# Kernel optimization log

Measured on AMD Instinct MI355X. Metric: run time of the kernel, lower is better.

Reference implementation:

```python
import jax, jax.numpy as jnp
import numpy as np

B, T, V, E, H = 256, 512, 30000, 256, 32


def _run_dir(x, mask, Wih, Whh, bih, bhh, reverse):
    # x: [B,T,D], mask: [B,T] bool. PyTorch GRU gate order: r, z, n.
    gi = jnp.einsum('btd,gd->btg', x, Wih) + bih  # precompute input gates [B,T,3H]
    h0 = jnp.zeros((x.shape[0], Whh.shape[1]), x.dtype)

    def step(h, inp):
        gi_t, m_t = inp
        gh = h @ Whh.T + bhh
        ir, iz, inn = jnp.split(gi_t, 3, axis=-1)
        hr, hz, hn = jnp.split(gh, 3, axis=-1)
        r = jax.nn.sigmoid(ir + hr)
        z = jax.nn.sigmoid(iz + hz)
        n = jnp.tanh(inn + r * hn)
        h_new = (1.0 - z) * n + z * h
        # packed-sequence semantics: freeze state at padded steps
        h = jnp.where(m_t[:, None], h_new, h)
        return h, h

    hT, ys = jax.lax.scan(step, h0, (jnp.swapaxes(gi, 0, 1), mask.T), reverse=reverse)
    return jnp.swapaxes(ys, 0, 1), hT  # outputs [B,T,H], final hidden [B,H]


def _bigru_layer(x, mask, pf, pb):
    of, hf = _run_dir(x, mask, *pf, reverse=False)
    ob, hb = _run_dir(x, mask, *pb, reverse=True)
    return jnp.concatenate([of, ob], axis=-1), hf, hb


def setup_inputs() -> dict:
    key = jax.random.key(0)
    ks = jax.random.split(key, 24)
    lengths = jax.random.randint(ks[0], (B,), 1, T + 1)
    mask = (jnp.arange(T)[None, :] < lengths[:, None]).astype(jnp.int32)
    ids = jax.random.randint(ks[1], (B, T), 1, V)
    ids = jnp.where(mask > 0, ids, 0)  # pad_id = 0 at padded positions
    embed = (jax.random.normal(ks[2], (V, E), jnp.float32) * 0.1).at[0].set(0.0)

    def gru_params(k, din):
        k1, k2, k3, k4 = jax.random.split(k, 4)
        s = 1.0 / np.sqrt(H)
        return (jax.random.uniform(k1, (3 * H, din), jnp.float32, -s, s),
                jax.random.uniform(k2, (3 * H, H), jnp.float32, -s, s),
                jax.random.uniform(k3, (3 * H,), jnp.float32, -s, s),
                jax.random.uniform(k4, (3 * H,), jnp.float32, -s, s))

    inp = {"input_ids": ids, "attention_mask": mask, "embed": embed}
    i = 3
    for layer, din in (("l0", E), ("l1", 2 * H)):
        for d in ("f", "b"):
            Wih, Whh, bih, bhh = gru_params(ks[i], din); i += 1
            inp[f"Wih_{layer}{d}"] = Wih
            inp[f"Whh_{layer}{d}"] = Whh
            inp[f"bih_{layer}{d}"] = bih
            inp[f"bhh_{layer}{d}"] = bhh
    s = 1.0 / np.sqrt(2 * H)
    inp["Wout"] = jax.random.uniform(ks[i], (6, 2 * H), jnp.float32, -s, s)
    inp["bout"] = jax.random.uniform(ks[i + 1], (6,), jnp.float32, -s, s)
    return inp


def reference(input_ids, attention_mask, embed,
              Wih_l0f, Whh_l0f, bih_l0f, bhh_l0f,
              Wih_l0b, Whh_l0b, bih_l0b, bhh_l0b,
              Wih_l1f, Whh_l1f, bih_l1f, bhh_l1f,
              Wih_l1b, Whh_l1b, bih_l1b, bhh_l1b,
              Wout, bout):
    mask = attention_mask > 0
    x = embed[input_ids]  # [B,T,E]
    x1, _, _ = _bigru_layer(x, mask,
                            (Wih_l0f, Whh_l0f, bih_l0f, bhh_l0f),
                            (Wih_l0b, Whh_l0b, bih_l0b, bhh_l0b))
    # no dropout: eval-mode forward
    _, hf, hb = _bigru_layer(x1, mask,
                             (Wih_l1f, Whh_l1f, bih_l1f, bhh_l1f),
                             (Wih_l1b, Whh_l1b, bih_l1b, bhh_l1b))
    top = jnp.concatenate([hf, hb], axis=-1)  # h_n[-2:] -> [B, 2H]
    return top @ Wout.T + bout  # [B, 6]
```

## Files before the change

### kernel.cpp

```cpp
#include <hip/hip_runtime.h>
#include <hip/hip_bf16.h>
#include <stdint.h>

#define B_ 256
#define T_ 512
#define V_ 30000
#define E_ 256
#define H_ 32

typedef float v2f __attribute__((ext_vector_type(2)));
typedef unsigned int uint2e __attribute__((ext_vector_type(2)));

#define LOG2E_F 1.44269504088896340736f

__device__ __forceinline__ float exp2_fast(float x) {
    float r; asm("v_exp_f32 %0, %1" : "=v"(r) : "v"(x)); return r;
}
__device__ __forceinline__ float rcp_fast(float x) {
    float r; asm("v_rcp_f32 %0, %1" : "=v"(r) : "v"(x)); return r;
}
__device__ __forceinline__ void pk_fma(v2f& acc, v2f w, v2f h) {
    asm("v_pk_fma_f32 %0, %1, %2, %0" : "+v"(acc) : "v"(w), "v"(h));
}
template <int CTRL>
__device__ __forceinline__ float mdpp(float x) {
    return __int_as_float(
        __builtin_amdgcn_mov_dpp(__float_as_int(x), CTRL, 0xF, 0xF, true));
}
#define DPP_XOR1  0xB1
#define DPP_XOR2  0x4E
#define DPP_XOR3  0x1B
#define DPP_XOR7  0x141
#define DPP_XOR15 0x140

__device__ __forceinline__ float xsum32(float x) {
    uint2e r = __builtin_amdgcn_permlane32_swap(
        __float_as_uint(x), __float_as_uint(x), false, false);
    return __uint_as_float(r.x) + __uint_as_float(r.y);
}
__device__ __forceinline__ float swap16(float x) {
    uint2e r = __builtin_amdgcn_permlane16_swap(
        __float_as_uint(x), __float_as_uint(x), false, false);
    return __uint_as_float(r.x ^ r.y ^ __float_as_uint(x));
}

#define GEMM_MT 64
#define GEMM_KC 32
#define GEMM_PA 68
#define GEMM_PB 196

__global__ __launch_bounds__(256) void gemm_gates(
    const float* __restrict__ A, int M, int K,
    const float* __restrict__ Wf, const float* __restrict__ Wb,
    const float* __restrict__ bihf, const float* __restrict__ bhhf,
    const float* __restrict__ bihb, const float* __restrict__ bhhb,
    float* __restrict__ Out)
{
    __shared__ float As[GEMM_KC][GEMM_PA];
    __shared__ float Bs[GEMM_KC][GEMM_PB];

    const int tid = threadIdx.x;
    const int mbase = blockIdx.x * GEMM_MT;
    const int mg = tid >> 5, ng = tid & 31;
    const int m_off = mg * 8, n_off = ng * 6;

    float acc[8][6];
    #pragma unroll
    for (int r = 0; r < 8; ++r)
        #pragma unroll
        for (int c = 0; c < 6; ++c) acc[r][c] = 0.f;

    for (int kc = 0; kc < K; kc += GEMM_KC) {
        #pragma unroll
        for (int i = 0; i < 2; ++i) {
            int fi = tid + 256 * i;
            int row = fi >> 3, cf = fi & 7;
            int m = mbase + row;
            float4 v = make_float4(0.f, 0.f, 0.f, 0.f);
            if (m < M) v = *(const float4*)&A[(size_t)m * K + kc + cf * 4];
            As[cf * 4 + 0][row] = v.x; As[cf * 4 + 1][row] = v.y;
            As[cf * 4 + 2][row] = v.z; As[cf * 4 + 3][row] = v.w;
        }
        #pragma unroll
        for (int i = 0; i < 6; ++i) {
            int fi = tid + 256 * i;
            int g = fi >> 3, cf = fi & 7;
            const float* Wsel = (g < 96) ? (Wf + (size_t)g * K)
                                         : (Wb + (size_t)(g - 96) * K);
            float4 v = *(const float4*)&Wsel[kc + cf * 4];
            Bs[cf * 4 + 0][g] = v.x; Bs[cf * 4 + 1][g] = v.y;
            Bs[cf * 4 + 2][g] = v.z; Bs[cf * 4 + 3][g] = v.w;
        }
        __syncthreads();
        #pragma unroll
        for (int k = 0; k < GEMM_KC; ++k) {
            float a[8], bb[6];
            *(float4*)&a[0] = *(const float4*)&As[k][m_off];
            *(float4*)&a[4] = *(const float4*)&As[k][m_off + 4];
            *(float2*)&bb[0] = *(const float2*)&Bs[k][n_off];
            *(float2*)&bb[2] = *(const float2*)&Bs[k][n_off + 2];
            *(float2*)&bb[4] = *(const float2*)&Bs[k][n_off + 4];
            #pragma unroll
            for (int r = 0; r < 8; ++r)
                #pragma unroll
                for (int c = 0; c < 6; ++c)
                    acc[r][c] = fmaf(a[r], bb[c], acc[r][c]);
        }
        __syncthreads();
    }

    float bias[6], gsc[6];
    #pragma unroll
    for (int c = 0; c < 6; ++c) {
        int g = n_off + c;
        int g96 = (g < 96) ? g : g - 96;
        const float* bih = (g < 96) ? bihf : bihb;
        const float* bhh = (g < 96) ? bhhf : bhhb;
        bias[c] = bih[g96] + ((g96 < 64) ? bhh[g96] : 0.f);
        gsc[c]  = (g96 < 64) ? -LOG2E_F : 2.0f * LOG2E_F;
    }
    #pragma unroll
    for (int r = 0; r < 8; ++r) {
        int m = mbase + m_off + r;
        if (m < M) {
            float* op = &Out[(size_t)m * 192 + n_off];
            #pragma unroll
            for (int c = 0; c < 6; ++c) op[c] = (acc[r][c] + bias[c]) * gsc[c];
        }
    }
}

template <int USE_IDS>
__global__ __launch_bounds__(64, 1)
__attribute__((amdgpu_waves_per_eu(1, 1)))
void gru_scan(
    const float* __restrict__ gi,
    const int* __restrict__ ids,
    const int* __restrict__ mask,
    const float* __restrict__ Whh_f, const float* __restrict__ Whh_b,
    const float* __restrict__ bhh_f, const float* __restrict__ bhh_b,
    float* __restrict__ out_seq,
    float* __restrict__ out_fin)
{
    const int l = threadIdx.x;
    const int i16 = l & 15;
    const int row = l >> 4;
    const int hi = row & 1;
    const int kh = row >> 1;
    const int j = i16 + 16 * hi;
    const bool lower = l < 32;
    const bool self_seed = (hi == kh);
    const int dir = blockIdx.x & 1;
    const int b = blockIdx.x >> 1;
    const int bT = b * T_;

    const float* Whh = dir ? Whh_b : Whh_f;
    const float* bhh = dir ? bhh_b : bhh_f;

    const float sRZ = -LOG2E_F;
    const float sN2 = 2.0f * LOG2E_F;

    const int M0[8] = {0, 2, 7, 5, 15, 13, 8, 10};
    const int M1[8] = {1, 3, 6, 4, 14, 12, 9, 11};

    v2f wR[8], wZ[8], wN[8];
    #pragma unroll
    for (int q = 0; q < 8; ++q) {
        const int c0 = kh * 16 + (i16 ^ M0[q]);
        const int c1 = kh * 16 + (i16 ^ M1[q]);
        wR[q] = (v2f){Whh[j * 32 + c0] * sRZ, Whh[j * 32 + c1] * sRZ};
        wZ[q] = (v2f){Whh[(32 + j) * 32 + c0] * sRZ,
                      Whh[(32 + j) * 32 + c1] * sRZ};
        wN[q] = (v2f){Whh[(64 + j) * 32 + c0] * sN2,
                      Whh[(64 + j) * 32 + c1] * sN2};
    }
    float bns = bhh[64 + j] * sN2;

    #pragma unroll
    for (int q = 0; q < 8; ++q)
        asm volatile("" : "+v"(wR[q]), "+v"(wZ[q]), "+v"(wN[q]));
    asm volatile("" : "+v"(bns));

    const int offR = dir * 96 + j;

    auto t_of = [&](int n) { return dir ? (T_ - 1 - n) : n; };
    auto cbase = [&](int c) { return dir ? (bT + 510 - 2 * c) : (bT + 2 * c); };

    int mk_cur = lower ? mask[bT + t_of(l)] : 0;
    int mk_nxt = lower ? mask[bT + t_of(32 + l)] : 0;

    int2 ids_pf = make_int2(0, 0), ids_in = make_int2(0, 0);
    float gR[2][2], gZ[2][2], gN[2][2];
    {
        int ra, rb;
        if (USE_IDS) {
            const int2 i0 = *(const int2*)&ids[cbase(0)];
            ra = dir ? i0.y : i0.x;
            rb = dir ? i0.x : i0.y;
            ids_pf = *(const int2*)&ids[cbase(1)];
        } else {
            ra = bT + t_of(0);
            rb = bT + t_of(1);
        }
        const float* ga = gi + (size_t)ra * 192 + offR;
        const float* gb = gi + (size_t)rb * 192 + offR;
        gR[0][0] = ga[0]; gZ[0][0] = ga[32]; gN[0][0] = ga[64];
        gR[0][1] = gb[0]; gZ[0][1] = gb[32]; gN[0][1] = gb[64];
    }

    float h = 0.f;

    for (int seg = 0; seg < 16; ++seg) {
        #pragma unroll
        for (int q = 0; q < 8; ++q)
            asm volatile("" : "+v"(wR[q]), "+v"(wZ[q]), "+v"(wN[q]));

        const uint32_t mseg = (uint32_t)__ballot(mk_cur != 0);
        mk_cur = mk_nxt;
        {
            const int ms = (seg + 2 < 16) ? (seg + 2) : 15;
            mk_nxt = lower ? mask[bT + t_of(32 * ms + l)] : 0;
        }

        for (int ch2 = 0; ch2 < 8; ++ch2) {
            const int cc0 = seg * 16 + 2 * ch2;
            #pragma unroll
            for (int pb = 0; pb < 2; ++pb) {
                const int cc = cc0 + pb;
                if (USE_IDS) {
                    const int ci = (cc + 2 < 256) ? (cc + 2) : 255;
                    ids_in = *(const int2*)&ids[cbase(ci)];
                }
                {
                    int ra, rb;
                    if (USE_IDS) {
                        ra = dir ? ids_pf.y : ids_pf.x;
                        rb = dir ? ids_pf.x : ids_pf.y;
                    } else {
                        const int cg = (cc + 1 < 256) ? (cc + 1) : 255;
                        ra = bT + t_of(2 * cg);
                        rb = bT + t_of(2 * cg + 1);
                    }
                    const float* ga = gi + (size_t)ra * 192 + offR;
                    const float* gb = gi + (size_t)rb * 192 + offR;
                    gR[pb ^ 1][0] = ga[0]; gZ[pb ^ 1][0] = ga[32]; gN[pb ^ 1][0] = ga[64];
                    gR[pb ^ 1][1] = gb[0]; gZ[pb ^ 1][1] = gb[32]; gN[pb ^ 1][1] = gb[64];
                }

                #pragma unroll
                for (int u = 0; u < 2; ++u) {
                    const int su = 4 * ch2 + 2 * pb + u;

                    const float hx = swap16(h);
                    const float seed = self_seed ? h : hx;

                    v2f p[8];
                    p[0].x = seed;                      p[0].y = mdpp<DPP_XOR1>(seed);
                    p[1].x = mdpp<DPP_XOR2>(seed);      p[1].y = mdpp<DPP_XOR3>(seed);
                    p[2].x = mdpp<DPP_XOR7>(seed);      p[2].y = mdpp<DPP_XOR7>(p[0].y);
                    p[3].x = mdpp<DPP_XOR7>(p[1].x);    p[3].y = mdpp<DPP_XOR7>(p[1].y);
                    p[4].x = mdpp<DPP_XOR15>(seed);     p[4].y = mdpp<DPP_XOR15>(p[0].y);
                    p[5].x = mdpp<DPP_XOR15>(p[1].x);   p[5].y = mdpp<DPP_XOR15>(p[1].y);
                    p[6].x = mdpp<DPP_XOR15>(p[2].x);   p[6].y = mdpp<DPP_XOR15>(p[2].y);
                    p[7].x = mdpp<DPP_XOR15>(p[3].x);   p[7].y = mdpp<DPP_XOR15>(p[3].y);

                    v2f aR0 = {0.f, 0.f}, aZ0 = {0.f, 0.f}, aN0 = {0.f, 0.f};
                    v2f aR1 = {0.f, 0.f}, aZ1 = {0.f, 0.f}, aN1 = {0.f, 0.f};
                    #pragma unroll
                    for (int q = 0; q < 4; ++q) {
                        pk_fma(aR0, wR[q], p[q]);
                        pk_fma(aZ0, wZ[q], p[q]);
                        pk_fma(aN0, wN[q], p[q]);
                    }
                    #pragma unroll
                    for (int q = 4; q < 8; ++q) {
                        pk_fma(aR1, wR[q], p[q]);
                        pk_fma(aZ1, wZ[q], p[q]);
                        pk_fma(aN1, wN[q], p[q]);
                    }
                    const v2f aR = aR0 + aR1;
                    const v2f aZ = aZ0 + aZ1;
                    const v2f aN = aN0 + aN1;

                    const float SR = xsum32(aR.x + aR.y);
                    const float SZ = xsum32(aZ.x + aZ.y);
                    const float SN = xsum32(aN.x + aN.y);

                    const float yr  = gR[pb][u] + SR;
                    const float yz  = gZ[pb][u] + SZ;
                    const float hns = bns + SN;
                    const float r = rcp_fast(1.0f + exp2_fast(yr));
                    const float z = rcp_fast(1.0f + exp2_fast(yz));
                    const float yn = fmaf(r, hns, gN[pb][u]);
                    const float n = fmaf(-2.0f, rcp_fast(1.0f + exp2_fast(yn)), 1.0f);
                    const float hnew = n + z * (h - n);
                    const bool mm = (mseg >> su) & 1u;
                    h = mm ? hnew : h;

                    if (out_seq != nullptr && lower) {
                        const int t = t_of(32 * seg + su);
                        out_seq[(size_t)(bT + t) * 64 + dir * 32 + j] = h;
                    }
                }
                if (USE_IDS) ids_pf = ids_in;
            }
        }
    }

    if (out_fin != nullptr && lower)
        out_fin[b * 64 + dir * 32 + j] = h;
}

__global__ void head_kernel(const float* __restrict__ hfin,
                            const float* __restrict__ Wout,
                            const float* __restrict__ bout,
                            float* __restrict__ out)
{
    int idx = blockIdx.x * blockDim.x + threadIdx.x;
    if (idx >= B_ * 6) return;
    int b = idx / 6, o = idx % 6;
    float acc = bout[o];
    const float* hp = hfin + b * 64;
    const float* wp = Wout + o * 64;
    #pragma unroll
    for (int k = 0; k < 64; ++k) acc = fmaf(hp[k], wp[k], acc);
    out[idx] = acc;
}

extern "C" void kernel_launch(void* const* d_in, const int* in_sizes, int n_in,
                              void* d_out, int out_size, void* d_ws, size_t ws_size,
                              hipStream_t stream)
{
    const int*   ids   = (const int*)d_in[0];
    const int*   mask  = (const int*)d_in[1];
    const float* embed = (const float*)d_in[2];
    const float* Wih0f = (const float*)d_in[3];
    const float* Whh0f = (const float*)d_in[4];
    const float* bih0f = (const float*)d_in[5];
    const float* bhh0f = (const float*)d_in[6];
    const float* Wih0b = (const float*)d_in[7];
    const float* Whh0b = (const float*)d_in[8];
    const float* bih0b = (const float*)d_in[9];
    const float* bhh0b = (const float*)d_in[10];
    const float* Wih1f = (const float*)d_in[11];
    const float* Whh1f = (const float*)d_in[12];
    const float* bih1f = (const float*)d_in[13];
    const float* bhh1f = (const float*)d_in[14];
    const float* Wih1b = (const float*)d_in[15];
    const float* Whh1b = (const float*)d_in[16];
    const float* bih1b = (const float*)d_in[17];
    const float* bhh1b = (const float*)d_in[18];
    const float* Wout  = (const float*)d_in[19];
    const float* bout  = (const float*)d_in[20];

    float* ws   = (float*)d_ws;
    float* gbuf = ws;
    float* x1   = ws + (size_t)B_ * T_ * 192;
    float* hfin = x1 + (size_t)B_ * T_ * 64;

    gemm_gates<<<(V_ + GEMM_MT - 1) / GEMM_MT, 256, 0, stream>>>(
        embed, V_, E_, Wih0f, Wih0b, bih0f, bhh0f, bih0b, bhh0b, gbuf);

    gru_scan<1><<<2 * B_, 64, 0, stream>>>(
        gbuf, ids, mask, Whh0f, Whh0b, bhh0f, bhh0b, x1, nullptr);

    gemm_gates<<<(B_ * T_) / GEMM_MT, 256, 0, stream>>>(
        x1, B_ * T_, 64, Wih1f, Wih1b, bih1f, bhh1f, bih1b, bhh1b, gbuf);

    gru_scan<0><<<2 * B_, 64, 0, stream>>>(
        gbuf, nullptr, mask, Whh1f, Whh1b, bhh1f, bhh1b, nullptr, hfin);

    head_kernel<<<(B_ * 6 + 255) / 256, 256, 0, stream>>>(hfin, Wout, bout,
                                                          (float*)d_out);
}
```

Baseline: 469.2 us.

## Interleave two batch sequences per wave in GRU scan for latency hiding

Measured after the change: 661.3 us. 1.41x slower.

```diff
diff --git a/kernel.cpp b/kernel.cpp
--- a/kernel.cpp
+++ b/kernel.cpp
@@ -151,8 +151,9 @@
     const bool lower = l < 32;
     const bool self_seed = (hi == kh);
     const int dir = blockIdx.x & 1;
-    const int b = blockIdx.x >> 1;
-    const int bT = b * T_;
+    const int bp = blockIdx.x >> 1;
+    const int b0T = (2 * bp) * T_;
+    const int b1T = (2 * bp + 1) * T_;
 
     const float* Whh = dir ? Whh_b : Whh_f;
     const float* bhh = dir ? bhh_b : bhh_f;
@@ -184,42 +185,101 @@
     const int offR = dir * 96 + j;
 
     auto t_of = [&](int n) { return dir ? (T_ - 1 - n) : n; };
-    auto cbase = [&](int c) { return dir ? (bT + 510 - 2 * c) : (bT + 2 * c); };
-
-    int mk_cur = lower ? mask[bT + t_of(l)] : 0;
-    int mk_nxt = lower ? mask[bT + t_of(32 + l)] : 0;
-
-    int2 ids_pf = make_int2(0, 0), ids_in = make_int2(0, 0);
-    float gR[2][2], gZ[2][2], gN[2][2];
+    auto cb0 = [&](int c) { return dir ? (b0T + 510 - 2 * c) : (b0T + 2 * c); };
+    auto cb1 = [&](int c) { return dir ? (b1T + 510 - 2 * c) : (b1T + 2 * c); };
+
+    auto step = [&](float h, float cR, float cZ, float cN, bool mm) -> float {
+        const float hx = swap16(h);
+        const float seed = self_seed ? h : hx;
+        v2f p[8];
+        p[0].x = seed;                      p[0].y = mdpp<DPP_XOR1>(seed);
+        p[1].x = mdpp<DPP_XOR2>(seed);      p[1].y = mdpp<DPP_XOR3>(seed);
+        p[2].x = mdpp<DPP_XOR7>(seed);      p[2].y = mdpp<DPP_XOR7>(p[0].y);
+        p[3].x = mdpp<DPP_XOR7>(p[1].x);    p[3].y = mdpp<DPP_XOR7>(p[1].y);
+        p[4].x = mdpp<DPP_XOR15>(seed);     p[4].y = mdpp<DPP_XOR15>(p[0].y);
+        p[5].x = mdpp<DPP_XOR15>(p[1].x);   p[5].y = mdpp<DPP_XOR15>(p[1].y);
+        p[6].x = mdpp<DPP_XOR15>(p[2].x);   p[6].y = mdpp<DPP_XOR15>(p[2].y);
+        p[7].x = mdpp<DPP_XOR15>(p[3].x);   p[7].y = mdpp<DPP_XOR15>(p[3].y);
+
+        v2f aR0 = {0.f, 0.f}, aZ0 = {0.f, 0.f}, aN0 = {0.f, 0.f};
+        v2f aR1 = {0.f, 0.f}, aZ1 = {0.f, 0.f}, aN1 = {0.f, 0.f};
+        #pragma unroll
+        for (int q = 0; q < 4; ++q) {
+            pk_fma(aR0, wR[q], p[q]);
+            pk_fma(aZ0, wZ[q], p[q]);
+            pk_fma(aN0, wN[q], p[q]);
+        }
+        #pragma unroll
+        for (int q = 4; q < 8; ++q) {
+            pk_fma(aR1, wR[q], p[q]);
+            pk_fma(aZ1, wZ[q], p[q]);
+            pk_fma(aN1, wN[q], p[q]);
+        }
+        const v2f aR = aR0 + aR1;
+        const v2f aZ = aZ0 + aZ1;
+        const v2f aN = aN0 + aN1;
+
+        const float SR = xsum32(aR.x + aR.y);
+        const float SZ = xsum32(aZ.x + aZ.y);
+        const float SN = xsum32(aN.x + aN.y);
+
+        const float yr  = cR + SR;
+        const float yz  = cZ + SZ;
+        const float hns = bns + SN;
+        const float r = rcp_fast(1.0f + exp2_fast(yr));
+        const float z = rcp_fast(1.0f + exp2_fast(yz));
+        const float yn = fmaf(r, hns, cN);
+        const float n = fmaf(-2.0f, rcp_fast(1.0f + exp2_fast(yn)), 1.0f);
+        const float hnew = n + z * (h - n);
+        return mm ? hnew : h;
+    };
+
+    int mkA_c = lower ? mask[b0T + t_of(l)] : 0;
+    int mkA_n = lower ? mask[b0T + t_of(32 + l)] : 0;
+    int mkB_c = lower ? mask[b1T + t_of(l)] : 0;
+    int mkB_n = lower ? mask[b1T + t_of(32 + l)] : 0;
+
+    int2 pfA = make_int2(0, 0), inA = make_int2(0, 0);
+    int2 pfB = make_int2(0, 0), inB = make_int2(0, 0);
+    float gAR[2][2], gAZ[2][2], gAN[2][2];
+    float gBR[2][2], gBZ[2][2], gBN[2][2];
     {
-        int ra, rb;
+        int raA, rbA, raB, rbB;
         if (USE_IDS) {
-            const int2 i0 = *(const int2*)&ids[cbase(0)];
-            ra = dir ? i0.y : i0.x;
-            rb = dir ? i0.x : i0.y;
-            ids_pf = *(const int2*)&ids[cbase(1)];
+            const int2 iA = *(const int2*)&ids[cb0(0)];
+            const int2 iB = *(const int2*)&ids[cb1(0)];
+            raA = dir ? iA.y : iA.x;  rbA = dir ? iA.x : iA.y;
+            raB = dir ? iB.y : iB.x;  rbB = dir ? iB.x : iB.y;
+            pfA = *(const int2*)&ids[cb0(1)];
+            pfB = *(const int2*)&ids[cb1(1)];
         } else {
-            ra = bT + t_of(0);
-            rb = bT + t_of(1);
-        }
-        const float* ga = gi + (size_t)ra * 192 + offR;
-        const float* gb = gi + (size_t)rb * 192 + offR;
-        gR[0][0] = ga[0]; gZ[0][0] = ga[32]; gN[0][0] = ga[64];
-        gR[0][1] = gb[0]; gZ[0][1] = gb[32]; gN[0][1] = gb[64];
-    }
-
-    float h = 0.f;
+            raA = b0T + t_of(0);  rbA = b0T + t_of(1);
+            raB = b1T + t_of(0);  rbB = b1T + t_of(1);
+        }
+        const float* ga = gi + (size_t)raA * 192 + offR;
+        const float* gb = gi + (size_t)rbA * 192 + offR;
+        gAR[0][0] = ga[0]; gAZ[0][0] = ga[32]; gAN[0][0] = ga[64];
+        gAR[0][1] = gb[0]; gAZ[0][1] = gb[32]; gAN[0][1] = gb[64];
+        const float* gc = gi + (size_t)raB * 192 + offR;
+        const float* gd = gi + (size_t)rbB * 192 + offR;
+        gBR[0][0] = gc[0]; gBZ[0][0] = gc[32]; gBN[0][0] = gc[64];
+        gBR[0][1] = gd[0]; gBZ[0][1] = gd[32]; gBN[0][1] = gd[64];
+    }
+
+    float h0 = 0.f, h1 = 0.f;
 
     for (int seg = 0; seg < 16; ++seg) {
         #pragma unroll
         for (int q = 0; q < 8; ++q)
             asm volatile("" : "+v"(wR[q]), "+v"(wZ[q]), "+v"(wN[q]));
 
-        const uint32_t mseg = (uint32_t)__ballot(mk_cur != 0);
-        mk_cur = mk_nxt;
+        const uint32_t msA = (uint32_t)__ballot(mkA_c != 0);
+        const uint32_t msB = (uint32_t)__ballot(mkB_c != 0);
+        mkA_c = mkA_n; mkB_c = mkB_n;
         {
             const int ms = (seg + 2 < 16) ? (seg + 2) : 15;
-            mk_nxt = lower ? mask[bT + t_of(32 * ms + l)] : 0;
+            mkA_n = lower ? mask[b0T + t_of(32 * ms + l)] : 0;
+            mkB_n = lower ? mask[b1T + t_of(32 * ms + l)] : 0;
         }
 
         for (int ch2 = 0; ch2 < 8; ++ch2) {
@@ -229,86 +289,55 @@
                 const int cc = cc0 + pb;
                 if (USE_IDS) {
                     const int ci = (cc + 2 < 256) ? (cc + 2) : 255;
-                    ids_in = *(const int2*)&ids[cbase(ci)];
+                    inA = *(const int2*)&ids[cb0(ci)];
+                    inB = *(const int2*)&ids[cb1(ci)];
                 }
                 {
-                    int ra, rb;
+                    int raA, rbA, raB, rbB;
                     if (USE_IDS) {
-                        ra = dir ? ids_pf.y : ids_pf.x;
-                        rb = dir ? ids_pf.x : ids_pf.y;
+                        raA = dir ? pfA.y : pfA.x;  rbA = dir ? pfA.x : pfA.y;
+                        raB = dir ? pfB.y : pfB.x;  rbB = dir ? pfB.x : pfB.y;
                     } else {
                         const int cg = (cc + 1 < 256) ? (cc + 1) : 255;
-                        ra = bT + t_of(2 * cg);
-                        rb = bT + t_of(2 * cg + 1);
+                        raA = b0T + t_of(2 * cg);  rbA = b0T + t_of(2 * cg + 1);
+                        raB = b1T + t_of(2 * cg);  rbB = b1T + t_of(2 * cg + 1);
                     }
-                    const float* ga = gi + (size_t)ra * 192 + offR;
-                    const float* gb = gi + (size_t)rb * 192 + offR;
-                    gR[pb ^ 1][0] = ga[0]; gZ[pb ^ 1][0] = ga[32]; gN[pb ^ 1][0] = ga[64];
-                    gR[pb ^ 1][1] = gb[0]; gZ[pb ^ 1][1] = gb[32]; gN[pb ^ 1][1] = gb[64];
+                    const float* ga = gi + (size_t)raA * 192 + offR;
+                    const float* gb = gi + (size_t)rbA * 192 + offR;
+                    gAR[pb ^ 1][0] = ga[0]; gAZ[pb ^ 1][0] = ga[32]; gAN[pb ^ 1][0] = ga[64];
+                    gAR[pb ^ 1][1] = gb[0]; gAZ[pb ^ 1][1] = gb[32]; gAN[pb ^ 1][1] = gb[64];
+                    const float* gc = gi + (size_t)raB * 192 + offR;
+                    const float* gd = gi + (size_t)rbB * 192 + offR;
+                    gBR[pb ^ 1][0] = gc[0]; gBZ[pb ^ 1][0] = gc[32]; gBN[pb ^ 1][0] = gc[64];
+                    gBR[pb ^ 1][1] = gd[0]; gBZ[pb ^ 1][1] = gd[32]; gBN[pb ^ 1][1] = gd[64];
                 }
 
                 #pragma unroll
                 for (int u = 0; u < 2; ++u) {
                     const int su = 4 * ch2 + 2 * pb + u;
 
-                    const float hx = swap16(h);
-                    const float seed = self_seed ? h : hx;
-
-                    v2f p[8];
-                    p[0].x = seed;                      p[0].y = mdpp<DPP_XOR1>(seed);
-                    p[1].x = mdpp<DPP_XOR2>(seed);      p[1].y = mdpp<DPP_XOR3>(seed);
-                    p[2].x = mdpp<DPP_XOR7>(seed);      p[2].y = mdpp<DPP_XOR7>(p[0].y);
-                    p[3].x = mdpp<DPP_XOR7>(p[1].x);    p[3].y = mdpp<DPP_XOR7>(p[1].y);
-                    p[4].x = mdpp<DPP_XOR15>(seed);     p[4].y = mdpp<DPP_XOR15>(p[0].y);
-                    p[5].x = mdpp<DPP_XOR15>(p[1].x);   p[5].y = mdpp<DPP_XOR15>(p[1].y);
-                    p[6].x = mdpp<DPP_XOR15>(p[2].x);   p[6].y = mdpp<DPP_XOR15>(p[2].y);
-                    p[7].x = mdpp<DPP_XOR15>(p[3].x);   p[7].y = mdpp<DPP_XOR15>(p[3].y);
-
-                    v2f aR0 = {0.f, 0.f}, aZ0 = {0.f, 0.f}, aN0 = {0.f, 0.f};
-                    v2f aR1 = {0.f, 0.f}, aZ1 = {0.f, 0.f}, aN1 = {0.f, 0.f};
-                    #pragma unroll
-                    for (int q = 0; q < 4; ++q) {
-                        pk_fma(aR0, wR[q], p[q]);
-                        pk_fma(aZ0, wZ[q], p[q]);
-                        pk_fma(aN0, wN[q], p[q]);
-                    }
-                    #pragma unroll
-                    for (int q = 4; q < 8; ++q) {
-                        pk_fma(aR1, wR[q], p[q]);
-                        pk_fma(aZ1, wZ[q], p[q]);
-                        pk_fma(aN1, wN[q], p[q]);
-                    }
-                    const v2f aR = aR0 + aR1;
-                    const v2f aZ = aZ0 + aZ1;
-                    const v2f aN = aN0 + aN1;
-
-                    const float SR = xsum32(aR.x + aR.y);
-                    const float SZ = xsum32(aZ.x + aZ.y);
-                    const float SN = xsum32(aN.x + aN.y);
-
-                    const float yr  = gR[pb][u] + SR;
-                    const float yz  = gZ[pb][u] + SZ;
-                    const float hns = bns + SN;
-                    const float r = rcp_fast(1.0f + exp2_fast(yr));
-                    const float z = rcp_fast(1.0f + exp2_fast(yz));
-                    const float yn = fmaf(r, hns, gN[pb][u]);
-                    const float n = fmaf(-2.0f, rcp_fast(1.0f + exp2_fast(yn)), 1.0f);
-                    const float hnew = n + z * (h - n);
-                    const bool mm = (mseg >> su) & 1u;
-                    h = mm ? hnew : h;
+                    const float nh0 = step(h0, gAR[pb][u], gAZ[pb][u],
+                                           gAN[pb][u], (msA >> su) & 1u);
+                    const float nh1 = step(h1, gBR[pb][u], gBZ[pb][u],
+                                           gBN[pb][u], (msB >> su) & 1u);
+                    h0 = nh0;
+                    h1 = nh1;
 
                     if (out_seq != nullptr && lower) {
                         const int t = t_of(32 * seg + su);
-                        out_seq[(size_t)(bT + t) * 64 + dir * 32 + j] = h;
+                        out_seq[(size_t)(b0T + t) * 64 + dir * 32 + j] = h0;
+                        out_seq[(size_t)(b1T + t) * 64 + dir * 32 + j] = h1;
                     }
                 }
-                if (USE_IDS) ids_pf = ids_in;
+                if (USE_IDS) { pfA = inA; pfB = inB; }
             }
         }
     }
 
-    if (out_fin != nullptr && lower)
-        out_fin[b * 64 + dir * 32 + j] = h;
+    if (out_fin != nullptr && lower) {
+        out_fin[(b0T / T_) * 64 + dir * 32 + j] = h0;
+        out_fin[(b1T / T_) * 64 + dir * 32 + j] = h1;
+    }
 }
 
 __global__ void head_kernel(const float* __restrict__ hfin,
@@ -361,13 +390,13 @@
     gemm_gates<<<(V_ + GEMM_MT - 1) / GEMM_MT, 256, 0, stream>>>(
         embed, V_, E_, Wih0f, Wih0b, bih0f, bhh0f, bih0b, bhh0b, gbuf);
 
-    gru_scan<1><<<2 * B_, 64, 0, stream>>>(
+    gru_scan<1><<<B_, 64, 0, stream>>>(
         gbuf, ids, mask, Whh0f, Whh0b, bhh0f, bhh0b, x1, nullptr);
 
     gemm_gates<<<(B_ * T_) / GEMM_MT, 256, 0, stream>>>(
         x1, B_ * T_, 64, Wih1f, Wih1b, bih1f, bhh1f, bih1b, bhh1b, gbuf);
 
-    gru_scan<0><<<2 * B_, 64, 0, stream>>>(
+    gru_scan<0><<<B_, 64, 0, stream>>>(
         gbuf, nullptr, mask, Whh1f, Whh1b, bhh1f, bhh1b, nullptr, hfin);
 
     head_kernel<<<(B_ * 6 + 255) / 256, 256, 0, stream>>>(hfin, Wout, bout,
```

## Split GRU recurrence across two waves sharing hidden state through LDS

Applied to the files above, without the earlier changes.

New measurement: 552.9 us. 1.18x slower.

```diff
diff --git a/kernel.cpp b/kernel.cpp
--- a/kernel.cpp
+++ b/kernel.cpp
@@ -22,26 +22,15 @@
 __device__ __forceinline__ void pk_fma(v2f& acc, v2f w, v2f h) {
     asm("v_pk_fma_f32 %0, %1, %2, %0" : "+v"(acc) : "v"(w), "v"(h));
 }
-template <int CTRL>
-__device__ __forceinline__ float mdpp(float x) {
-    return __int_as_float(
-        __builtin_amdgcn_mov_dpp(__float_as_int(x), CTRL, 0xF, 0xF, true));
-}
-#define DPP_XOR1  0xB1
-#define DPP_XOR2  0x4E
-#define DPP_XOR3  0x1B
-#define DPP_XOR7  0x141
-#define DPP_XOR15 0x140
-
 __device__ __forceinline__ float xsum32(float x) {
     uint2e r = __builtin_amdgcn_permlane32_swap(
         __float_as_uint(x), __float_as_uint(x), false, false);
     return __uint_as_float(r.x) + __uint_as_float(r.y);
 }
-__device__ __forceinline__ float swap16(float x) {
+__device__ __forceinline__ float xsum16(float x) {
     uint2e r = __builtin_amdgcn_permlane16_swap(
         __float_as_uint(x), __float_as_uint(x), false, false);
-    return __uint_as_float(r.x ^ r.y ^ __float_as_uint(x));
+    return __uint_as_float(r.x) + __uint_as_float(r.y);
 }
 
 #define GEMM_MT 64
@@ -131,8 +120,7 @@
 }
 
 template <int USE_IDS>
-__global__ __launch_bounds__(64, 1)
-__attribute__((amdgpu_waves_per_eu(1, 1)))
+__global__ __launch_bounds__(128, 1)
 void gru_scan(
     const float* __restrict__ gi,
     const int* __restrict__ ids,
@@ -142,14 +130,16 @@
     float* __restrict__ out_seq,
     float* __restrict__ out_fin)
 {
-    const int l = threadIdx.x;
+    __shared__ float hsh[2][32];
+
+    const int tid = threadIdx.x;
+    const int w = tid >> 6;
+    const int l = tid & 63;
     const int i16 = l & 15;
-    const int row = l >> 4;
-    const int hi = row & 1;
-    const int kh = row >> 1;
-    const int j = i16 + 16 * hi;
+    const int kq = l >> 4;
+    const int j = w * 16 + i16;
+    const bool lead = (kq == 0);
     const bool lower = l < 32;
-    const bool self_seed = (hi == kh);
     const int dir = blockIdx.x & 1;
     const int b = blockIdx.x >> 1;
     const int bT = b * T_;
@@ -160,24 +150,20 @@
     const float sRZ = -LOG2E_F;
     const float sN2 = 2.0f * LOG2E_F;
 
-    const int M0[8] = {0, 2, 7, 5, 15, 13, 8, 10};
-    const int M1[8] = {1, 3, 6, 4, 14, 12, 9, 11};
-
-    v2f wR[8], wZ[8], wN[8];
-    #pragma unroll
-    for (int q = 0; q < 8; ++q) {
-        const int c0 = kh * 16 + (i16 ^ M0[q]);
-        const int c1 = kh * 16 + (i16 ^ M1[q]);
-        wR[q] = (v2f){Whh[j * 32 + c0] * sRZ, Whh[j * 32 + c1] * sRZ};
-        wZ[q] = (v2f){Whh[(32 + j) * 32 + c0] * sRZ,
-                      Whh[(32 + j) * 32 + c1] * sRZ};
-        wN[q] = (v2f){Whh[(64 + j) * 32 + c0] * sN2,
-                      Whh[(64 + j) * 32 + c1] * sN2};
+    v2f wR[4], wZ[4], wN[4];
+    #pragma unroll
+    for (int q = 0; q < 4; ++q) {
+        const int k0 = 8 * kq + 2 * q;
+        wR[q] = (v2f){Whh[j * 32 + k0] * sRZ, Whh[j * 32 + k0 + 1] * sRZ};
+        wZ[q] = (v2f){Whh[(32 + j) * 32 + k0] * sRZ,
+                      Whh[(32 + j) * 32 + k0 + 1] * sRZ};
+        wN[q] = (v2f){Whh[(64 + j) * 32 + k0] * sN2,
+                      Whh[(64 + j) * 32 + k0 + 1] * sN2};
     }
     float bns = bhh[64 + j] * sN2;
 
     #pragma unroll
-    for (int q = 0; q < 8; ++q)
+    for (int q = 0; q < 4; ++q)
         asm volatile("" : "+v"(wR[q]), "+v"(wZ[q]), "+v"(wN[q]));
     asm volatile("" : "+v"(bns));
 
@@ -185,6 +171,8 @@
 
     auto t_of = [&](int n) { return dir ? (T_ - 1 - n) : n; };
     auto cbase = [&](int c) { return dir ? (bT + 510 - 2 * c) : (bT + 2 * c); };
+
+    if (tid < 32) { hsh[0][tid] = 0.f; hsh[1][tid] = 0.f; }
 
     int mk_cur = lower ? mask[bT + t_of(l)] : 0;
     int mk_nxt = lower ? mask[bT + t_of(32 + l)] : 0;
@@ -209,10 +197,11 @@
     }
 
     float h = 0.f;
+    __syncthreads();
 
     for (int seg = 0; seg < 16; ++seg) {
         #pragma unroll
-        for (int q = 0; q < 8; ++q)
+        for (int q = 0; q < 4; ++q)
             asm volatile("" : "+v"(wR[q]), "+v"(wZ[q]), "+v"(wN[q]));
 
         const uint32_t mseg = (uint32_t)__ballot(mk_cur != 0);
@@ -251,40 +240,22 @@
                 for (int u = 0; u < 2; ++u) {
                     const int su = 4 * ch2 + 2 * pb + u;
 
-                    const float hx = swap16(h);
-                    const float seed = self_seed ? h : hx;
-
-                    v2f p[8];
-                    p[0].x = seed;                      p[0].y = mdpp<DPP_XOR1>(seed);
-                    p[1].x = mdpp<DPP_XOR2>(seed);      p[1].y = mdpp<DPP_XOR3>(seed);
-                    p[2].x = mdpp<DPP_XOR7>(seed);      p[2].y = mdpp<DPP_XOR7>(p[0].y);
-                    p[3].x = mdpp<DPP_XOR7>(p[1].x);    p[3].y = mdpp<DPP_XOR7>(p[1].y);
-                    p[4].x = mdpp<DPP_XOR15>(seed);     p[4].y = mdpp<DPP_XOR15>(p[0].y);
-                    p[5].x = mdpp<DPP_XOR15>(p[1].x);   p[5].y = mdpp<DPP_XOR15>(p[1].y);
-                    p[6].x = mdpp<DPP_XOR15>(p[2].x);   p[6].y = mdpp<DPP_XOR15>(p[2].y);
-                    p[7].x = mdpp<DPP_XOR15>(p[3].x);   p[7].y = mdpp<DPP_XOR15>(p[3].y);
-
-                    v2f aR0 = {0.f, 0.f}, aZ0 = {0.f, 0.f}, aN0 = {0.f, 0.f};
-                    v2f aR1 = {0.f, 0.f}, aZ1 = {0.f, 0.f}, aN1 = {0.f, 0.f};
-                    #pragma unroll
-                    for (int q = 0; q < 4; ++q) {
-                        pk_fma(aR0, wR[q], p[q]);
-                        pk_fma(aZ0, wZ[q], p[q]);
-                        pk_fma(aN0, wN[q], p[q]);
-                    }
-                    #pragma unroll
-                    for (int q = 4; q < 8; ++q) {
-                        pk_fma(aR1, wR[q], p[q]);
-                        pk_fma(aZ1, wZ[q], p[q]);
-                        pk_fma(aN1, wN[q], p[q]);
-                    }
-                    const v2f aR = aR0 + aR1;
-                    const v2f aZ = aZ0 + aZ1;
-                    const v2f aN = aN0 + aN1;
-
-                    const float SR = xsum32(aR.x + aR.y);
-                    const float SZ = xsum32(aZ.x + aZ.y);
-                    const float SN = xsum32(aN.x + aN.y);
+                    const float4 s0 = *(const float4*)&hsh[u][8 * kq];
+                    const float4 s1 = *(const float4*)&hsh[u][8 * kq + 4];
+                    const v2f p0 = (v2f){s0.x, s0.y};
+                    const v2f p1 = (v2f){s0.z, s0.w};
+                    const v2f p2 = (v2f){s1.x, s1.y};
+                    const v2f p3 = (v2f){s1.z, s1.w};
+
+                    v2f aR = {0.f, 0.f}, aZ = {0.f, 0.f}, aN = {0.f, 0.f};
+                    pk_fma(aR, wR[0], p0); pk_fma(aZ, wZ[0], p0); pk_fma(aN, wN[0], p0);
+                    pk_fma(aR, wR[1], p1); pk_fma(aZ, wZ[1], p1); pk_fma(aN, wN[1], p1);
+                    pk_fma(aR, wR[2], p2); pk_fma(aZ, wZ[2], p2); pk_fma(aN, wN[2], p2);
+                    pk_fma(aR, wR[3], p3); pk_fma(aZ, wZ[3], p3); pk_fma(aN, wN[3], p3);
+
+                    const float SR = xsum16(xsum32(aR.x + aR.y));
+                    const float SZ = xsum16(xsum32(aZ.x + aZ.y));
+                    const float SN = xsum16(xsum32(aN.x + aN.y));
 
                     const float yr  = gR[pb][u] + SR;
                     const float yz  = gZ[pb][u] + SZ;
@@ -297,7 +268,10 @@
                     const bool mm = (mseg >> su) & 1u;
                     h = mm ? hnew : h;
 
-                    if (out_seq != nullptr && lower) {
+                    hsh[u ^ 1][j] = h;
+                    __syncthreads();
+
+                    if (out_seq != nullptr && lead) {
                         const int t = t_of(32 * seg + su);
                         out_seq[(size_t)(bT + t) * 64 + dir * 32 + j] = h;
                     }
@@ -307,7 +281,7 @@
         }
     }
 
-    if (out_fin != nullptr && lower)
+    if (out_fin != nullptr && lead)
         out_fin[b * 64 + dir * 32 + j] = h;
 }
 
@@ -361,13 +335,13 @@
     gemm_gates<<<(V_ + GEMM_MT - 1) / GEMM_MT, 256, 0, stream>>>(
         embed, V_, E_, Wih0f, Wih0b, bih0f, bhh0f, bih0b, bhh0b, gbuf);
 
-    gru_scan<1><<<2 * B_, 64, 0, stream>>>(
+    gru_scan<1><<<2 * B_, 128, 0, stream>>>(
         gbuf, ids, mask, Whh0f, Whh0b, bhh0f, bhh0b, x1, nullptr);
 
     gemm_gates<<<(B_ * T_) / GEMM_MT, 256, 0, stream>>>(
         x1, B_ * T_, 64, Wih1f, Wih1b, bih1f, bhh1f, bih1b, bhh1b, gbuf);
 
-    gru_scan<0><<<2 * B_, 64, 0, stream>>>(
+    gru_scan<0><<<2 * B_, 128, 0, stream>>>(
         gbuf, nullptr, mask, Whh1f, Whh1b, bhh1f, bhh1b, nullptr, hfin);
 
     head_kernel<<<(B_ * 6 + 255) / 256, 256, 0, stream>>>(hfin, Wout, bout,
```
